# Kernel tuning notes

Measured on AMD Instinct MI355X. Metric: run time of the kernel, lower is better.

The kernel has to match this reference:

```python
import jax, jax.numpy as jnp
import numpy as np

PAD = 0

def setup_inputs() -> dict:
    key = jax.random.key(0)
    k1, k2, k3, k4 = jax.random.split(key, 4)
    B, S, F, V, H, D = 64, 256, 4, 50257, 768, 512
    words = jax.random.randint(k1, (B, S, F), 0, V, dtype=jnp.int64)  # pad_index=0 occurs rarely at random
    E = jax.random.normal(k2, (V, H), dtype=jnp.float32) * 0.02      # stand-in for transformer last_hidden_state producer
    W = jax.random.normal(k3, (H, D), dtype=jnp.float32) * 0.02      # FFN projection weight
    b = jax.random.normal(k4, (D,), dtype=jnp.float32) * 0.02
    return {"words": words, "E": E, "W": W, "b": b}

def reference(words, E, W, b):
    # words: [B, S, F] subword ids; mask out pad subwords
    mask = (words != PAD)                                  # [B,S,F] bool
    sub = E[words] * mask[..., None].astype(E.dtype)       # [B,S,F,H], pads zeroed
    cnt = mask.sum(-1).astype(E.dtype)                     # [B,S] subwords per word
    # segment-mean over the fix_len axis; fully-padded words -> 0 (matches pad_sequence(..., 0))
    word_emb = sub.sum(-2) / jnp.maximum(cnt, 1.0)[..., None]   # [B,S,H]
    word_emb = jnp.where((cnt > 0)[..., None], word_emb, 0.0)
    return word_emb @ W + b                                # [B,S,D]
```

## Files before the change

### kernel.cpp

```cpp
#include <hip/hip_runtime.h>
#include <hip/hip_bf16.h>

#define M_TOT 16384
#define K_TOT 768
#define N_TOT 512
#define NT 12
#define NSLOT 96

typedef __attribute__((ext_vector_type(8))) __bf16 bf16x8;
typedef __attribute__((ext_vector_type(4))) float f32x4;

static __device__ __forceinline__ ushort f2bf(float x) {
  union { float f; unsigned int u; } v; v.f = x;
  unsigned int r = v.u + 0x7fffu + ((v.u >> 16) & 1u);
  return (ushort)(r >> 16);
}
static __device__ __forceinline__ unsigned pack2(float lo, float hi) {
  return (unsigned)f2bf(lo) | ((unsigned)f2bf(hi) << 16);
}

__global__ __launch_bounds__(256) void wt_kernel(const float* __restrict__ W,
                                                 ushort* __restrict__ Wt) {
  __shared__ float tile[64][65];
  const int t  = threadIdx.x;
  const int k0 = blockIdx.x * 64;
  const int n0 = blockIdx.y * 64;
#pragma unroll
  for (int i = 0; i < 4; ++i) {
    const int idx = t + i * 256;
    const int r = idx >> 4;
    const int c = (idx & 15) * 4;
    const float4 v =
        *reinterpret_cast<const float4*>(W + (size_t)(k0 + r) * N_TOT + n0 + c);
    tile[r][c + 0] = v.x; tile[r][c + 1] = v.y;
    tile[r][c + 2] = v.z; tile[r][c + 3] = v.w;
  }
  __syncthreads();
#pragma unroll
  for (int i = 0; i < 4; ++i) {
    const int idx = t + i * 256;
    const int rn = idx >> 4;
    const int ck = (idx & 15) * 4;
    ushort4 o;
    o.x = f2bf(tile[ck + 0][rn]);
    o.y = f2bf(tile[ck + 1][rn]);
    o.z = f2bf(tile[ck + 2][rn]);
    o.w = f2bf(tile[ck + 3][rn]);
    const int kg    = k0 + ck;
    const int chunk = kg >> 3;
    const int e0    = kg & 7;
    *reinterpret_cast<ushort4*>(
        &Wt[((size_t)chunk * N_TOT + n0 + rn) * 8 + e0]) = o;
  }
}

__global__ __launch_bounds__(512, 1) void fused_kernel(
    const int* __restrict__ words, const float* __restrict__ E,
    const ushort* __restrict__ Wt, const float* __restrict__ bias,
    float* __restrict__ out) {
  __shared__ ushort A0[32 * NSLOT * 8];
  __shared__ ushort A1[32 * NSLOT * 8];
  __shared__ int   eoff_l[64][4];
  __shared__ float msk_l[64][4];
  __shared__ float scl_l[64];

  const int t    = threadIdx.x;
  const int lane = t & 63;
  const int w    = t >> 6;
  const int bm   = blockIdx.x;

  if (t < 64) {
    const int4 w4 =
        *reinterpret_cast<const int4*>(words + (size_t)(bm * 64 + t) * 4);
    const int ids[4] = {w4.x, w4.y, w4.z, w4.w};
    float cnt = 0.f;
#pragma unroll
    for (int f = 0; f < 4; ++f) {
      eoff_l[t][f] = ids[f] * K_TOT;
      const float m = (ids[f] != 0) ? 1.f : 0.f;
      msk_l[t][f] = m;
      cnt += m;
    }
    scl_l[t] = (cnt > 0.f) ? (1.f / cnt) : 0.f;
  }
  __syncthreads();

  const int sr  = t >> 4;
  const int seg = t & 7;
  const int ktb = (t >> 3) & 1;
  const int sw  = seg ^ (sr & 7);

  const float4* pf[2][4];
#pragma unroll
  for (int f = 0; f < 4; ++f) {
    pf[0][f] = reinterpret_cast<const float4*>(E + eoff_l[sr][f] + seg * 8);
    pf[1][f] =
        reinterpret_cast<const float4*>(E + eoff_l[32 + sr][f] + seg * 8);
  }
  const float mk[2][4] = {
      {msk_l[sr][0], msk_l[sr][1], msk_l[sr][2], msk_l[sr][3]},
      {msk_l[32 + sr][0], msk_l[32 + sr][1], msk_l[32 + sr][2],
       msk_l[32 + sr][3]}};
  const float sc[2] = {scl_l[sr], scl_l[32 + sr]};

  float4 vgA[8], vgB[8];

#define G_LOAD(vg, S, g)                                                     \
  do {                                                                       \
    const int kt_ = 2 * (g) + ktb;                                           \
    _Pragma("unroll") for (int f = 0; f < 4; ++f) {                          \
      vg[2 * f + 0] = pf[S][f][kt_ * 16 + 0];                                \
      vg[2 * f + 1] = pf[S][f][kt_ * 16 + 1];                                \
    }                                                                        \
  } while (0)

#define G_MATH(vg, dst, S, g)                                                \
  do {                                                                       \
    const int kt_ = 2 * (g) + ktb;                                           \
    float s[8];                                                              \
    _Pragma("unroll") for (int j = 0; j < 4; ++j) {                          \
      s[j] = (vg[0][j] * mk[S][0] + vg[2][j] * mk[S][1] +                    \
              vg[4][j] * mk[S][2] + vg[6][j] * mk[S][3]) * sc[S];            \
      s[4 + j] = (vg[1][j] * mk[S][0] + vg[3][j] * mk[S][1] +                \
                  vg[5][j] * mk[S][2] + vg[7][j] * mk[S][3]) * sc[S];        \
    }                                                                        \
    uint4 o;                                                                 \
    o.x = pack2(s[0], s[1]); o.y = pack2(s[2], s[3]);                        \
    o.z = pack2(s[4], s[5]); o.w = pack2(s[6], s[7]);                        \
    *reinterpret_cast<uint4*>(&(dst)[(sr * NSLOT + kt_ * 8 + sw) * 8]) = o;  \
  } while (0)

  const int rsel = lane & 15;
  const int ksel = lane >> 4;
  const int colBase = w * 64 + rsel;

  f32x4 acc[2][4];

#define COMPUTE(Asrc, kt)                                                    \
  do {                                                                       \
    _Pragma("unroll") for (int kk = 0; kk < 2; ++kk) {                       \
      const int ks = kk * 4 + ksel;                                          \
      bf16x8 af[2], bfr[4];                                                  \
      _Pragma("unroll") for (int m = 0; m < 2; ++m) {                        \
        const int r = m * 16 + rsel;                                         \
        af[m] = *reinterpret_cast<const bf16x8*>(                            \
            &(Asrc)[(r * NSLOT + (kt) * 8 + (ks ^ (r & 7))) * 8]);           \
      }                                                                      \
      _Pragma("unroll") for (int n = 0; n < 4; ++n)                          \
        bfr[n] = *reinterpret_cast<const bf16x8*>(                           \
            &Wt[((size_t)((kt) * 8 + ks) * N_TOT + colBase + n * 16) * 8]);  \
      _Pragma("unroll") for (int m = 0; m < 2; ++m)                          \
        _Pragma("unroll") for (int n = 0; n < 4; ++n)                        \
          acc[m][n] = __builtin_amdgcn_mfma_f32_16x16x32_bf16(               \
              af[m], bfr[n], acc[m][n], 0, 0, 0);                            \
    }                                                                        \
  } while (0)

#define EPILOGUE(T)                                                          \
  do {                                                                       \
    const int row0 = bm * 64 + (T) * 32 + (ksel << 2);                       \
    _Pragma("unroll") for (int n = 0; n < 4; ++n) {                          \
      const float bv = bias[colBase + n * 16];                               \
      _Pragma("unroll") for (int m = 0; m < 2; ++m) {                        \
        _Pragma("unroll") for (int j = 0; j < 4; ++j) {                      \
          __builtin_nontemporal_store(                                       \
              acc[m][n][j] + bv,                                             \
              &out[(size_t)(row0 + m * 16 + j) * N_TOT + colBase + n * 16]); \
        }                                                                    \
      }                                                                      \
    }                                                                        \
  } while (0)

  G_LOAD(vgA, 0, 0);
  G_LOAD(vgB, 0, 1);
  G_MATH(vgA, A0, 0, 0);  G_LOAD(vgA, 0, 2);
  G_MATH(vgB, A0, 0, 1);  G_LOAD(vgB, 0, 3);
  G_MATH(vgA, A0, 0, 2);  G_LOAD(vgA, 0, 4);
  G_MATH(vgB, A0, 0, 3);  G_LOAD(vgB, 0, 5);
  G_MATH(vgA, A0, 0, 4);
  G_MATH(vgB, A0, 0, 5);
  __syncthreads();

#pragma unroll
  for (int m = 0; m < 2; ++m)
#pragma unroll
    for (int n = 0; n < 4; ++n) acc[m][n] = (f32x4){0.f, 0.f, 0.f, 0.f};

  G_LOAD(vgA, 1, 0);
  COMPUTE(A0, 0);
  COMPUTE(A0, 1);
  G_LOAD(vgB, 1, 1);
  COMPUTE(A0, 2);
  G_MATH(vgA, A1, 1, 0);
  COMPUTE(A0, 3);
  G_LOAD(vgA, 1, 2);
  COMPUTE(A0, 4);
  G_MATH(vgB, A1, 1, 1);
  COMPUTE(A0, 5);
  G_LOAD(vgB, 1, 3);
  COMPUTE(A0, 6);
  G_MATH(vgA, A1, 1, 2);
  COMPUTE(A0, 7);
  G_LOAD(vgA, 1, 4);
  COMPUTE(A0, 8);
  G_MATH(vgB, A1, 1, 3);
  COMPUTE(A0, 9);
  G_LOAD(vgB, 1, 5);
  COMPUTE(A0, 10);
  G_MATH(vgA, A1, 1, 4);
  COMPUTE(A0, 11);
  G_MATH(vgB, A1, 1, 5);

  EPILOGUE(0);
  __syncthreads();

#pragma unroll
  for (int m = 0; m < 2; ++m)
#pragma unroll
    for (int n = 0; n < 4; ++n) acc[m][n] = (f32x4){0.f, 0.f, 0.f, 0.f};
#pragma unroll
  for (int kt = 0; kt < NT; ++kt) COMPUTE(A1, kt);
  EPILOGUE(1);

#undef G_LOAD
#undef G_MATH
#undef COMPUTE
#undef EPILOGUE
}

extern "C" void kernel_launch(void* const* d_in, const int* in_sizes, int n_in,
                              void* d_out, int out_size, void* d_ws,
                              size_t ws_size, hipStream_t stream) {
  const int*   words = (const int*)d_in[0];
  const float* E     = (const float*)d_in[1];
  const float* W     = (const float*)d_in[2];
  const float* b     = (const float*)d_in[3];
  float* out = (float*)d_out;

  ushort* Wtws = (ushort*)d_ws;

  hipLaunchKernelGGL(wt_kernel, dim3(K_TOT / 64, N_TOT / 64), dim3(256), 0,
                     stream, W, Wtws);
  hipLaunchKernelGGL(fused_kernel, dim3(M_TOT / 64), dim3(512), 0, stream,
                     words, E, Wtws, b, out);
}
```

Measured before the change: 54.21 us.

## Warp-specialize fused kernel into gather producer and MFMA consumer waves

Splits the 8 waves per block into 4 producer waves that gather, mask-average and pack embedding rows into LDS, and 4 consumer waves that run the MFMA GEMM over 128 columns each. Synchronization uses block barriers, with matching __syncthreads counts on both branches. Consumers raise wave priority around the MFMA bursts. The aim is to overlap gather latency with matrix math. In exchange, each consumer doubles its accumulator registers, and the gather work is now done by half as many threads.

```diff
diff --git a/kernel.cpp b/kernel.cpp
--- a/kernel.cpp
+++ b/kernel.cpp
@@ -64,10 +64,9 @@
   __shared__ float msk_l[64][4];
   __shared__ float scl_l[64];
 
-  const int t    = threadIdx.x;
-  const int lane = t & 63;
-  const int w    = t >> 6;
-  const int bm   = blockIdx.x;
+  const int t  = threadIdx.x;
+  const int w  = t >> 6;
+  const int bm = blockIdx.x;
 
   if (t < 64) {
     const int4 w4 =
@@ -85,38 +84,36 @@
   }
   __syncthreads();
 
-  const int sr  = t >> 4;
-  const int seg = t & 7;
-  const int ktb = (t >> 3) & 1;
-  const int sw  = seg ^ (sr & 7);
-
-  const float4* pf[2][4];
-#pragma unroll
-  for (int f = 0; f < 4; ++f) {
-    pf[0][f] = reinterpret_cast<const float4*>(E + eoff_l[sr][f] + seg * 8);
-    pf[1][f] =
-        reinterpret_cast<const float4*>(E + eoff_l[32 + sr][f] + seg * 8);
-  }
-  const float mk[2][4] = {
-      {msk_l[sr][0], msk_l[sr][1], msk_l[sr][2], msk_l[sr][3]},
-      {msk_l[32 + sr][0], msk_l[32 + sr][1], msk_l[32 + sr][2],
-       msk_l[32 + sr][3]}};
-  const float sc[2] = {scl_l[sr], scl_l[32 + sr]};
-
-  float4 vgA[8], vgB[8];
-
-#define G_LOAD(vg, S, g)                                                     \
-  do {                                                                       \
-    const int kt_ = 2 * (g) + ktb;                                           \
+  if (w < 4) {
+    const int sr  = t >> 3;
+    const int seg = t & 7;
+    const int sw  = seg ^ (sr & 7);
+
+    const float4* pf[2][4];
+#pragma unroll
+    for (int f = 0; f < 4; ++f) {
+      pf[0][f] = reinterpret_cast<const float4*>(E + eoff_l[sr][f] + seg * 8);
+      pf[1][f] =
+          reinterpret_cast<const float4*>(E + eoff_l[32 + sr][f] + seg * 8);
+    }
+    const float mk[2][4] = {
+        {msk_l[sr][0], msk_l[sr][1], msk_l[sr][2], msk_l[sr][3]},
+        {msk_l[32 + sr][0], msk_l[32 + sr][1], msk_l[32 + sr][2],
+         msk_l[32 + sr][3]}};
+    const float sc[2] = {scl_l[sr], scl_l[32 + sr]};
+
+    float4 vgA[8], vgB[8];
+
+#define P_LOAD(vg, S, kt)                                                    \
+  do {                                                                       \
     _Pragma("unroll") for (int f = 0; f < 4; ++f) {                          \
-      vg[2 * f + 0] = pf[S][f][kt_ * 16 + 0];                                \
-      vg[2 * f + 1] = pf[S][f][kt_ * 16 + 1];                                \
-    }                                                                        \
-  } while (0)
-
-#define G_MATH(vg, dst, S, g)                                                \
-  do {                                                                       \
-    const int kt_ = 2 * (g) + ktb;                                           \
+      vg[2 * f + 0] = pf[S][f][(kt) * 16 + 0];                               \
+      vg[2 * f + 1] = pf[S][f][(kt) * 16 + 1];                               \
+    }                                                                        \
+  } while (0)
+
+#define P_MATH(vg, dst, S, kt)                                               \
+  do {                                                                       \
     float s[8];                                                              \
     _Pragma("unroll") for (int j = 0; j < 4; ++j) {                          \
       s[j] = (vg[0][j] * mk[S][0] + vg[2][j] * mk[S][1] +                    \
@@ -127,39 +124,75 @@
     uint4 o;                                                                 \
     o.x = pack2(s[0], s[1]); o.y = pack2(s[2], s[3]);                        \
     o.z = pack2(s[4], s[5]); o.w = pack2(s[6], s[7]);                        \
-    *reinterpret_cast<uint4*>(&(dst)[(sr * NSLOT + kt_ * 8 + sw) * 8]) = o;  \
-  } while (0)
-
-  const int rsel = lane & 15;
-  const int ksel = lane >> 4;
-  const int colBase = w * 64 + rsel;
-
-  f32x4 acc[2][4];
-
-#define COMPUTE(Asrc, kt)                                                    \
+    *reinterpret_cast<uint4*>(&(dst)[(sr * NSLOT + (kt) * 8 + sw) * 8]) = o; \
+  } while (0)
+
+    P_LOAD(vgA, 0, 0);      P_LOAD(vgB, 0, 1);
+    P_MATH(vgA, A0, 0, 0);  P_LOAD(vgA, 0, 2);
+    P_MATH(vgB, A0, 0, 1);  P_LOAD(vgB, 0, 3);
+    P_MATH(vgA, A0, 0, 2);  P_LOAD(vgA, 0, 4);
+    P_MATH(vgB, A0, 0, 3);  P_LOAD(vgB, 0, 5);
+    P_MATH(vgA, A0, 0, 4);  P_LOAD(vgA, 0, 6);
+    P_MATH(vgB, A0, 0, 5);  P_LOAD(vgB, 0, 7);
+    P_MATH(vgA, A0, 0, 6);  P_LOAD(vgA, 0, 8);
+    P_MATH(vgB, A0, 0, 7);  P_LOAD(vgB, 0, 9);
+    P_MATH(vgA, A0, 0, 8);  P_LOAD(vgA, 0, 10);
+    P_MATH(vgB, A0, 0, 9);  P_LOAD(vgB, 0, 11);
+    P_MATH(vgA, A0, 0, 10);
+    P_MATH(vgB, A0, 0, 11);
+    __syncthreads();
+
+    P_LOAD(vgA, 1, 0);      P_LOAD(vgB, 1, 1);
+    P_MATH(vgA, A1, 1, 0);  P_LOAD(vgA, 1, 2);
+    P_MATH(vgB, A1, 1, 1);  P_LOAD(vgB, 1, 3);
+    P_MATH(vgA, A1, 1, 2);  P_LOAD(vgA, 1, 4);
+    P_MATH(vgB, A1, 1, 3);  P_LOAD(vgB, 1, 5);
+    P_MATH(vgA, A1, 1, 4);  P_LOAD(vgA, 1, 6);
+    P_MATH(vgB, A1, 1, 5);  P_LOAD(vgB, 1, 7);
+    P_MATH(vgA, A1, 1, 6);  P_LOAD(vgA, 1, 8);
+    P_MATH(vgB, A1, 1, 7);  P_LOAD(vgB, 1, 9);
+    P_MATH(vgA, A1, 1, 8);  P_LOAD(vgA, 1, 10);
+    P_MATH(vgB, A1, 1, 9);  P_LOAD(vgB, 1, 11);
+    P_MATH(vgA, A1, 1, 10);
+    P_MATH(vgB, A1, 1, 11);
+    __syncthreads();
+#undef P_LOAD
+#undef P_MATH
+  } else {
+    const int lane = t & 63;
+    const int cw   = w - 4;
+    const int rsel = lane & 15;
+    const int ksel = lane >> 4;
+    const int colBase = cw * 128 + rsel;
+
+    f32x4 acc[2][8];
+
+#define C_COMPUTE(Asrc, kt)                                                  \
   do {                                                                       \
     _Pragma("unroll") for (int kk = 0; kk < 2; ++kk) {                       \
       const int ks = kk * 4 + ksel;                                          \
-      bf16x8 af[2], bfr[4];                                                  \
+      bf16x8 af[2], bfr[8];                                                  \
       _Pragma("unroll") for (int m = 0; m < 2; ++m) {                        \
         const int r = m * 16 + rsel;                                         \
         af[m] = *reinterpret_cast<const bf16x8*>(                            \
             &(Asrc)[(r * NSLOT + (kt) * 8 + (ks ^ (r & 7))) * 8]);           \
       }                                                                      \
-      _Pragma("unroll") for (int n = 0; n < 4; ++n)                          \
+      _Pragma("unroll") for (int n = 0; n < 8; ++n)                          \
         bfr[n] = *reinterpret_cast<const bf16x8*>(                           \
             &Wt[((size_t)((kt) * 8 + ks) * N_TOT + colBase + n * 16) * 8]);  \
+      __builtin_amdgcn_s_setprio(1);                                         \
       _Pragma("unroll") for (int m = 0; m < 2; ++m)                          \
-        _Pragma("unroll") for (int n = 0; n < 4; ++n)                        \
+        _Pragma("unroll") for (int n = 0; n < 8; ++n)                        \
           acc[m][n] = __builtin_amdgcn_mfma_f32_16x16x32_bf16(               \
               af[m], bfr[n], acc[m][n], 0, 0, 0);                            \
-    }                                                                        \
-  } while (0)
-
-#define EPILOGUE(T)                                                          \
+      __builtin_amdgcn_s_setprio(0);                                         \
+    }                                                                        \
+  } while (0)
+
+#define C_EPILOGUE(T)                                                        \
   do {                                                                       \
     const int row0 = bm * 64 + (T) * 32 + (ksel << 2);                       \
-    _Pragma("unroll") for (int n = 0; n < 4; ++n) {                          \
+    _Pragma("unroll") for (int n = 0; n < 8; ++n) {                          \
       const float bv = bias[colBase + n * 16];                               \
       _Pragma("unroll") for (int m = 0; m < 2; ++m) {                        \
         _Pragma("unroll") for (int j = 0; j < 4; ++j) {                      \
@@ -171,61 +204,25 @@
     }                                                                        \
   } while (0)
 
-  G_LOAD(vgA, 0, 0);
-  G_LOAD(vgB, 0, 1);
-  G_MATH(vgA, A0, 0, 0);  G_LOAD(vgA, 0, 2);
-  G_MATH(vgB, A0, 0, 1);  G_LOAD(vgB, 0, 3);
-  G_MATH(vgA, A0, 0, 2);  G_LOAD(vgA, 0, 4);
-  G_MATH(vgB, A0, 0, 3);  G_LOAD(vgB, 0, 5);
-  G_MATH(vgA, A0, 0, 4);
-  G_MATH(vgB, A0, 0, 5);
-  __syncthreads();
-
-#pragma unroll
-  for (int m = 0; m < 2; ++m)
-#pragma unroll
-    for (int n = 0; n < 4; ++n) acc[m][n] = (f32x4){0.f, 0.f, 0.f, 0.f};
-
-  G_LOAD(vgA, 1, 0);
-  COMPUTE(A0, 0);
-  COMPUTE(A0, 1);
-  G_LOAD(vgB, 1, 1);
-  COMPUTE(A0, 2);
-  G_MATH(vgA, A1, 1, 0);
-  COMPUTE(A0, 3);
-  G_LOAD(vgA, 1, 2);
-  COMPUTE(A0, 4);
-  G_MATH(vgB, A1, 1, 1);
-  COMPUTE(A0, 5);
-  G_LOAD(vgB, 1, 3);
-  COMPUTE(A0, 6);
-  G_MATH(vgA, A1, 1, 2);
-  COMPUTE(A0, 7);
-  G_LOAD(vgA, 1, 4);
-  COMPUTE(A0, 8);
-  G_MATH(vgB, A1, 1, 3);
-  COMPUTE(A0, 9);
-  G_LOAD(vgB, 1, 5);
-  COMPUTE(A0, 10);
-  G_MATH(vgA, A1, 1, 4);
-  COMPUTE(A0, 11);
-  G_MATH(vgB, A1, 1, 5);
-
-  EPILOGUE(0);
-  __syncthreads();
-
-#pragma unroll
-  for (int m = 0; m < 2; ++m)
-#pragma unroll
-    for (int n = 0; n < 4; ++n) acc[m][n] = (f32x4){0.f, 0.f, 0.f, 0.f};
-#pragma unroll
-  for (int kt = 0; kt < NT; ++kt) COMPUTE(A1, kt);
-  EPILOGUE(1);
-
-#undef G_LOAD
-#undef G_MATH
-#undef COMPUTE
-#undef EPILOGUE
+    __syncthreads();
+#pragma unroll
+    for (int m = 0; m < 2; ++m)
+#pragma unroll
+      for (int n = 0; n < 8; ++n) acc[m][n] = (f32x4){0.f, 0.f, 0.f, 0.f};
+#pragma unroll
+    for (int kt = 0; kt < NT; ++kt) C_COMPUTE(A0, kt);
+    C_EPILOGUE(0);
+    __syncthreads();
+#pragma unroll
+    for (int m = 0; m < 2; ++m)
+#pragma unroll
+      for (int n = 0; n < 8; ++n) acc[m][n] = (f32x4){0.f, 0.f, 0.f, 0.f};
+#pragma unroll
+    for (int kt = 0; kt < NT; ++kt) C_COMPUTE(A1, kt);
+    C_EPILOGUE(1);
+#undef C_COMPUTE
+#undef C_EPILOGUE
+  }
 }
 
 extern "C" void kernel_launch(void* const* d_in, const int* in_sizes, int n_in,
```

Measured after the change: 107.1 us. +97.5%, slower.

## Gather whole embedding rows per wave and batch loads around MFMA phases

Applied to the files above, without the earlier changes.

Changes the gather mapping so each wave loads four full 768-float embedding rows, with lanes reading contiguous float4s, instead of each thread covering 16-float segments across many rows. The loads are grouped into two large batches that overlap six MFMA compute steps each, fenced with sched_barriers. s_setprio is raised around the MFMA bursts. The aim is more coalesced, larger gather transactions and fewer scheduling interleavings, at the cost of more live registers (24 float4 buffers).

```diff
diff --git a/kernel.cpp b/kernel.cpp
--- a/kernel.cpp
+++ b/kernel.cpp
@@ -5,7 +5,6 @@
 #define K_TOT 768
 #define N_TOT 512
 #define NT 12
-#define NSLOT 96
 
 typedef __attribute__((ext_vector_type(8))) __bf16 bf16x8;
 typedef __attribute__((ext_vector_type(4))) float f32x4;
@@ -58,8 +57,8 @@
     const int* __restrict__ words, const float* __restrict__ E,
     const ushort* __restrict__ Wt, const float* __restrict__ bias,
     float* __restrict__ out) {
-  __shared__ ushort A0[32 * NSLOT * 8];
-  __shared__ ushort A1[32 * NSLOT * 8];
+  __shared__ ushort A0[32 * 96 * 8];
+  __shared__ ushort A1[32 * 96 * 8];
   __shared__ int   eoff_l[64][4];
   __shared__ float msk_l[64][4];
   __shared__ float scl_l[64];
@@ -68,11 +67,12 @@
   const int lane = t & 63;
   const int w    = t >> 6;
   const int bm   = blockIdx.x;
+  const int w4   = w * 4;
 
   if (t < 64) {
-    const int4 w4 =
+    const int4 wd =
         *reinterpret_cast<const int4*>(words + (size_t)(bm * 64 + t) * 4);
-    const int ids[4] = {w4.x, w4.y, w4.z, w4.w};
+    const int ids[4] = {wd.x, wd.y, wd.z, wd.w};
     float cnt = 0.f;
 #pragma unroll
     for (int f = 0; f < 4; ++f) {
@@ -85,74 +85,64 @@
   }
   __syncthreads();
 
-  const int sr  = t >> 4;
-  const int seg = t & 7;
-  const int ktb = (t >> 3) & 1;
-  const int sw  = seg ^ (sr & 7);
-
-  const float4* pf[2][4];
-#pragma unroll
-  for (int f = 0; f < 4; ++f) {
-    pf[0][f] = reinterpret_cast<const float4*>(E + eoff_l[sr][f] + seg * 8);
-    pf[1][f] =
-        reinterpret_cast<const float4*>(E + eoff_l[32 + sr][f] + seg * 8);
-  }
-  const float mk[2][4] = {
-      {msk_l[sr][0], msk_l[sr][1], msk_l[sr][2], msk_l[sr][3]},
-      {msk_l[32 + sr][0], msk_l[32 + sr][1], msk_l[32 + sr][2],
-       msk_l[32 + sr][3]}};
-  const float sc[2] = {scl_l[sr], scl_l[32 + sr]};
-
-  float4 vgA[8], vgB[8];
-
-#define G_LOAD(vg, S, g)                                                     \
-  do {                                                                       \
-    const int kt_ = 2 * (g) + ktb;                                           \
+  float4 vA[12], vB[12];
+
+#define G_LOAD(vv, grow)                                                     \
+  do {                                                                       \
+    const int row_ = (grow);                                                 \
     _Pragma("unroll") for (int f = 0; f < 4; ++f) {                          \
-      vg[2 * f + 0] = pf[S][f][kt_ * 16 + 0];                                \
-      vg[2 * f + 1] = pf[S][f][kt_ * 16 + 1];                                \
-    }                                                                        \
-  } while (0)
-
-#define G_MATH(vg, dst, S, g)                                                \
-  do {                                                                       \
-    const int kt_ = 2 * (g) + ktb;                                           \
-    float s[8];                                                              \
-    _Pragma("unroll") for (int j = 0; j < 4; ++j) {                          \
-      s[j] = (vg[0][j] * mk[S][0] + vg[2][j] * mk[S][1] +                    \
-              vg[4][j] * mk[S][2] + vg[6][j] * mk[S][3]) * sc[S];            \
-      s[4 + j] = (vg[1][j] * mk[S][0] + vg[3][j] * mk[S][1] +                \
-                  vg[5][j] * mk[S][2] + vg[7][j] * mk[S][3]) * sc[S];        \
-    }                                                                        \
-    uint4 o;                                                                 \
-    o.x = pack2(s[0], s[1]); o.y = pack2(s[2], s[3]);                        \
-    o.z = pack2(s[4], s[5]); o.w = pack2(s[6], s[7]);                        \
-    *reinterpret_cast<uint4*>(&(dst)[(sr * NSLOT + kt_ * 8 + sw) * 8]) = o;  \
+      const float4* p_ =                                                     \
+          reinterpret_cast<const float4*>(E + eoff_l[row_][f]) + lane;       \
+      vv[f * 3 + 0] = p_[0];                                                 \
+      vv[f * 3 + 1] = p_[64];                                                \
+      vv[f * 3 + 2] = p_[128];                                               \
+    }                                                                        \
+  } while (0)
+
+#define G_MATH(vv, grow, dstA, lrow)                                         \
+  do {                                                                       \
+    const int row_ = (grow);                                                 \
+    const float km0 = msk_l[row_][0], km1 = msk_l[row_][1];                  \
+    const float km2 = msk_l[row_][2], km3 = msk_l[row_][3];                  \
+    const float ksc = scl_l[row_];                                           \
+    _Pragma("unroll") for (int c = 0; c < 3; ++c) {                          \
+      float s[4];                                                            \
+      _Pragma("unroll") for (int j = 0; j < 4; ++j)                          \
+        s[j] = (vv[0 * 3 + c][j] * km0 + vv[1 * 3 + c][j] * km1 +            \
+                vv[2 * 3 + c][j] * km2 + vv[3 * 3 + c][j] * km3) * ksc;      \
+      uint2 o_;                                                              \
+      o_.x = pack2(s[0], s[1]);                                              \
+      o_.y = pack2(s[2], s[3]);                                              \
+      const int slot_ = c * 32 + ((lane >> 1) ^ (row_ & 7));                 \
+      *reinterpret_cast<uint2*>(                                             \
+          &(dstA)[(lrow) * 768 + slot_ * 8 + (lane & 1) * 4]) = o_;          \
+    }                                                                        \
   } while (0)
 
   const int rsel = lane & 15;
   const int ksel = lane >> 4;
   const int colBase = w * 64 + rsel;
-
   f32x4 acc[2][4];
 
 #define COMPUTE(Asrc, kt)                                                    \
   do {                                                                       \
     _Pragma("unroll") for (int kk = 0; kk < 2; ++kk) {                       \
-      const int ks = kk * 4 + ksel;                                          \
+      const int g = (kt) * 8 + kk * 4 + ksel;                                \
       bf16x8 af[2], bfr[4];                                                  \
       _Pragma("unroll") for (int m = 0; m < 2; ++m) {                        \
-        const int r = m * 16 + rsel;                                         \
+        const int r_ = m * 16 + rsel;                                        \
         af[m] = *reinterpret_cast<const bf16x8*>(                            \
-            &(Asrc)[(r * NSLOT + (kt) * 8 + (ks ^ (r & 7))) * 8]);           \
+            &(Asrc)[r_ * 768 + ((g ^ (r_ & 7))) * 8]);                       \
       }                                                                      \
       _Pragma("unroll") for (int n = 0; n < 4; ++n)                          \
         bfr[n] = *reinterpret_cast<const bf16x8*>(                           \
-            &Wt[((size_t)((kt) * 8 + ks) * N_TOT + colBase + n * 16) * 8]);  \
+            &Wt[((size_t)g * N_TOT + colBase + n * 16) * 8]);                \
+      __builtin_amdgcn_s_setprio(1);                                         \
       _Pragma("unroll") for (int m = 0; m < 2; ++m)                          \
         _Pragma("unroll") for (int n = 0; n < 4; ++n)                        \
           acc[m][n] = __builtin_amdgcn_mfma_f32_16x16x32_bf16(               \
               af[m], bfr[n], acc[m][n], 0, 0, 0);                            \
+      __builtin_amdgcn_s_setprio(0);                                         \
     }                                                                        \
   } while (0)
 
@@ -171,14 +161,12 @@
     }                                                                        \
   } while (0)
 
-  G_LOAD(vgA, 0, 0);
-  G_LOAD(vgB, 0, 1);
-  G_MATH(vgA, A0, 0, 0);  G_LOAD(vgA, 0, 2);
-  G_MATH(vgB, A0, 0, 1);  G_LOAD(vgB, 0, 3);
-  G_MATH(vgA, A0, 0, 2);  G_LOAD(vgA, 0, 4);
-  G_MATH(vgB, A0, 0, 3);  G_LOAD(vgB, 0, 5);
-  G_MATH(vgA, A0, 0, 4);
-  G_MATH(vgB, A0, 0, 5);
+  G_LOAD(vA, w4 + 0);
+  G_LOAD(vB, w4 + 1);
+  G_MATH(vA, w4 + 0, A0, w4 + 0);  G_LOAD(vA, w4 + 2);
+  G_MATH(vB, w4 + 1, A0, w4 + 1);  G_LOAD(vB, w4 + 3);
+  G_MATH(vA, w4 + 2, A0, w4 + 2);
+  G_MATH(vB, w4 + 3, A0, w4 + 3);
   __syncthreads();
 
 #pragma unroll
@@ -186,31 +174,22 @@
 #pragma unroll
     for (int n = 0; n < 4; ++n) acc[m][n] = (f32x4){0.f, 0.f, 0.f, 0.f};
 
-  G_LOAD(vgA, 1, 0);
-  COMPUTE(A0, 0);
-  COMPUTE(A0, 1);
-  G_LOAD(vgB, 1, 1);
-  COMPUTE(A0, 2);
-  G_MATH(vgA, A1, 1, 0);
-  COMPUTE(A0, 3);
-  G_LOAD(vgA, 1, 2);
-  COMPUTE(A0, 4);
-  G_MATH(vgB, A1, 1, 1);
-  COMPUTE(A0, 5);
-  G_LOAD(vgB, 1, 3);
-  COMPUTE(A0, 6);
-  G_MATH(vgA, A1, 1, 2);
-  COMPUTE(A0, 7);
-  G_LOAD(vgA, 1, 4);
-  COMPUTE(A0, 8);
-  G_MATH(vgB, A1, 1, 3);
-  COMPUTE(A0, 9);
-  G_LOAD(vgB, 1, 5);
-  COMPUTE(A0, 10);
-  G_MATH(vgA, A1, 1, 4);
-  COMPUTE(A0, 11);
-  G_MATH(vgB, A1, 1, 5);
-
+  __builtin_amdgcn_sched_barrier(0);
+  G_LOAD(vA, 32 + w4 + 0);
+  G_LOAD(vB, 32 + w4 + 1);
+  __builtin_amdgcn_sched_barrier(0);
+  COMPUTE(A0, 0);  COMPUTE(A0, 1);  COMPUTE(A0, 2);
+  COMPUTE(A0, 3);  COMPUTE(A0, 4);  COMPUTE(A0, 5);
+  G_MATH(vA, 32 + w4 + 0, A1, w4 + 0);
+  G_MATH(vB, 32 + w4 + 1, A1, w4 + 1);
+  __builtin_amdgcn_sched_barrier(0);
+  G_LOAD(vA, 32 + w4 + 2);
+  G_LOAD(vB, 32 + w4 + 3);
+  __builtin_amdgcn_sched_barrier(0);
+  COMPUTE(A0, 6);  COMPUTE(A0, 7);  COMPUTE(A0, 8);
+  COMPUTE(A0, 9);  COMPUTE(A0, 10); COMPUTE(A0, 11);
+  G_MATH(vA, 32 + w4 + 2, A1, w4 + 2);
+  G_MATH(vB, 32 + w4 + 3, A1, w4 + 3);
   EPILOGUE(0);
   __syncthreads();
 
```

After: 56.81 us. 1.05x slower.
